# Performance work log

Hardware: AMD Instinct MI355X
Metric: run time of the kernel (lower is better)

Reference implementation:

```python
import jax, jax.numpy as jnp
import numpy as np

BATCH, SEQ, HEADS, EMB = 16, 4096, 16, 64
SHAPE = int(SEQ ** 0.5)          # 64 (2D grid side)
N = 2 * SHAPE - 1                # 127 (circular conv length)


def setup_inputs() -> dict:
    key = jax.random.key(0)
    k_v, k_w = jax.random.split(key)
    v = jax.random.normal(k_v, (BATCH, SEQ, HEADS, EMB), dtype=jnp.float32)
    # 'full' bias base: learned relative bias of length 2*shape_-1 per head
    w = jax.random.normal(k_w, (1, HEADS, N), dtype=jnp.float32)
    o_ = jnp.ones((SHAPE,), dtype=jnp.float32)
    return {"v": v, "w": w, "o_": o_}


def reference(v, w, o_):
    B, S, H, E = v.shape
    s = int(S ** 0.5)
    n = 2 * s - 1

    # bias_base_type == 'full': slice w[..., shape_-s : shape_+s-1] == all of w
    z_fft = jnp.fft.rfft(w)                              # (1, H, n//2+1) complex

    # v: [B, S, H, E] -> [B, E, H, s1, s2]
    vt = jnp.transpose(v, (0, 3, 2, 1)).reshape(B, E, H, s, s)
    v_s = vt.sum(axis=3)                                 # sum over s1 -> [B, E, H, s2]
    u_s = vt.sum(axis=4)                                 # sum over s2 -> [B, E, H, s1]

    pad = ((0, 0), (0, 0), (0, 0), (s - 1, 0))
    v_m_fft = jnp.fft.rfft(jnp.pad(v_s, pad))            # [B, E, H, n//2+1]
    u_m_fft = jnp.fft.rfft(jnp.pad(u_s, pad))

    zf = z_fft[:, None]                                  # (1, 1, H, n//2+1)
    RxV = jnp.fft.irfft(v_m_fft * zf, n=n)[..., :s]      # [B, E, H, s]
    RxU = jnp.fft.irfft(u_m_fft * zf, n=n)[..., :s]      # [B, E, H, s]

    # outer sum over the 2D grid, flatten back to seq
    pbv = RxV[..., None, :] + RxU[..., :, None]          # [B, E, H, s, s]
    pbv = pbv.reshape(B, E, H, S)
    pbv = jnp.transpose(pbv, (0, 3, 2, 1))               # [B, S, H, E]

    # normalizer term z_pb (batch independent)
    o_pad = jnp.pad(o_, ((s - 1, 0),))                   # (n,)
    o_fft = jnp.fft.rfft(o_pad)                          # (n//2+1,)
    z_pb = jnp.fft.irfft(o_fft * z_fft, n=n)[..., :s] * s  # (1, H, s)
    z_pb = z_pb[..., None, :] + z_pb[..., :, None]       # (1, H, s, s)
    z_pb = z_pb.reshape(-1, H, s * s)                    # (1, H, S)
    z_pb = jnp.transpose(z_pb, (0, 2, 1))                # (1, S, H)

    return pbv, z_pb
```

## Files before the change

### kernel.cpp

```cpp
#include <hip/hip_runtime.h>

#define BATCH 16
#define SEQ   4096
#define HEADS 16
#define EMB   64
#define SS    64
#define NW    127
#define PLANE (HEADS * EMB)

#define US_ELEMS    (BATCH * SS * PLANE)
#define VPART_ELEMS (BATCH * 4 * SS * PLANE)
#define WS_NEEDED ((size_t)(VPART_ELEMS + US_ELEMS) * sizeof(float))

__global__ __launch_bounds__(256) void sums_kernel(
    const float4* __restrict__ v4, float4* __restrict__ vpart4,
    float4* __restrict__ us4)
{
    __shared__ float4 u_lds[4][16][64];

    const int blk = blockIdx.x;
    const int b   = blk >> 4;
    const int q   = (blk >> 2) & 3;
    const int cq  = blk & 3;
    const int tid = threadIdx.x;
    const int w   = tid >> 6;
    const int c4  = tid & 63;

    const float4* base = v4 + (((size_t)(b * SEQ + q * 1024)) << 8)
                            + (cq << 6) + c4;

    float4 vacc[16];
    #pragma unroll
    for (int m = 0; m < 16; ++m) vacc[m] = make_float4(0.f, 0.f, 0.f, 0.f);

    for (int il = 0; il < 16; ++il) {
        float4 uacc = make_float4(0.f, 0.f, 0.f, 0.f);
        #pragma unroll
        for (int m = 0; m < 16; ++m) {
            const float4 x = base[(size_t)((il << 6) + w + (m << 2)) << 8];
            uacc.x += x.x; uacc.y += x.y; uacc.z += x.z; uacc.w += x.w;
            vacc[m].x += x.x; vacc[m].y += x.y;
            vacc[m].z += x.z; vacc[m].w += x.w;
        }
        u_lds[w][il][c4] = uacc;
    }
    __syncthreads();

    {
        int s = tid;
        #pragma unroll
        for (int r = 0; r < 4; ++r, s += 256) {
            const int il = s >> 6, c = s & 63;
            float4 a = u_lds[0][il][c];
            #pragma unroll
            for (int ww = 1; ww < 4; ++ww) {
                const float4 x = u_lds[ww][il][c];
                a.x += x.x; a.y += x.y; a.z += x.z; a.w += x.w;
            }
            us4[((size_t)((b << 6) + (q << 4) + il) << 8) + (cq << 6) + c] = a;
        }
    }

    #pragma unroll
    for (int m = 0; m < 16; ++m) {
        const int j = w + (m << 2);
        vpart4[((size_t)((((b << 2) + q) << 6) + j) << 8) + (cq << 6) + c4]
            = vacc[m];
    }
}

__global__ __launch_bounds__(512) void convexp_kernel(
    const float* __restrict__ w, const float4* __restrict__ vpart4,
    const float4* __restrict__ us4, float* __restrict__ out)
{
    __shared__ float wtab[NW];
    __shared__ float vsl[SS][SS];
    __shared__ float usl[SS][SS];

    const int bh   = blockIdx.x;
    const int b    = bh >> 4;
    const int h    = bh & (HEADS - 1);
    const int tid  = threadIdx.x;
    const int wave = tid >> 6;
    const int lane = tid & 63;

    if (tid < NW) wtab[tid] = w[h * NW + tid];

    for (int s = tid; s < SS * 16; s += 512) {
        const int j = s >> 4, e4 = s & 15;
        float4 acc = make_float4(0.f, 0.f, 0.f, 0.f);
        #pragma unroll
        for (int q = 0; q < 4; ++q) {
            const float4 x =
                vpart4[((size_t)((((b << 2) + q) << 6) + j) << 8) + (h << 4) + e4];
            acc.x += x.x; acc.y += x.y; acc.z += x.z; acc.w += x.w;
        }
        *(float4*)&vsl[j][e4 << 2] = acc;
        *(float4*)&usl[j][e4 << 2] =
            us4[((size_t)((b << 6) + j) << 8) + (h << 4) + e4];
    }
    __syncthreads();

    const int t0 = wave << 3;
    float accv[8], accu[8];
    #pragma unroll
    for (int tt = 0; tt < 8; ++tt) { accv[tt] = 0.0f; accu[tt] = 0.0f; }

    #pragma unroll
    for (int jb = 0; jb < 4; ++jb) {
        float wreg[23];
        #pragma unroll
        for (int d = 0; d < 23; ++d) {
            int idx = t0 - (jb << 4) + 49 + d;
            if (idx >= NW) idx -= NW;
            wreg[d] = wtab[idx];
        }
        #pragma unroll
        for (int jj = 0; jj < 16; ++jj) {
            const float cv = vsl[(jb << 4) + jj][lane];
            const float cu = usl[(jb << 4) + jj][lane];
            #pragma unroll
            for (int tt = 0; tt < 8; ++tt) {
                const float cw = wreg[15 + tt - jj];
                accv[tt] += cw * cv;
                accu[tt] += cw * cu;
            }
        }
    }
    __syncthreads();
    #pragma unroll
    for (int tt = 0; tt < 8; ++tt) {
        vsl[t0 + tt][lane] = accv[tt];
        usl[t0 + tt][lane] = accu[tt];
    }
    __syncthreads();

    float* obase = out + (((size_t)b * SEQ) << 10) + (h << 6) + lane;
    for (int ii = 0; ii < 8; ++ii) {
        const int i = (wave << 3) + ii;
        const float ruv = usl[i][lane];
        #pragma unroll
        for (int j = 0; j < SS; ++j) {
            obase[(size_t)((i << 6) + j) << 10] = vsl[j][lane] + ruv;
        }
    }
}

__global__ __launch_bounds__(512) void pbv_kernel(const float* __restrict__ v,
                                                  const float* __restrict__ w,
                                                  float* __restrict__ out) {
    __shared__ float us [SS][SS];
    __shared__ float vsf[SS][SS];
    __shared__ float wtab[NW];

    const int bh   = blockIdx.x;
    const int b    = bh / HEADS;
    const int h    = bh % HEADS;
    const int tid  = threadIdx.x;
    const int wave = tid >> 6;
    const int lane = tid & 63;

    for (int idx = tid; idx < SS * SS; idx += 512) (&vsf[0][0])[idx] = 0.0f;
    if (tid < NW) wtab[tid] = w[h * NW + tid];
    __syncthreads();

    const float* vbase = v + ((size_t)b * SEQ * HEADS + h) * EMB + lane;
    float vsacc[SS];
    #pragma unroll
    for (int j = 0; j < SS; ++j) vsacc[j] = 0.0f;

    for (int ii = 0; ii < 8; ++ii) {
        const int i = wave * 8 + ii;
        const float* rowp = vbase + (size_t)i * SS * (HEADS * EMB);
        float uacc = 0.0f;
        #pragma unroll
        for (int j = 0; j < SS; ++j) {
            float val = rowp[(size_t)j * (HEADS * EMB)];
            uacc += val;
            vsacc[j] += val;
        }
        us[i][lane] = uacc;
    }
    #pragma unroll
    for (int j = 0; j < SS; ++j) atomicAdd(&vsf[j][lane], vsacc[j]);
    __syncthreads();

    float rv[8], ru[8];
    for (int tt = 0; tt < 8; ++tt) {
        const int t = wave * 8 + tt;
        float accv = 0.0f, accu = 0.0f;
        #pragma unroll
        for (int j = 0; j < SS; ++j) {
            int k = t - j + 64;
            if (k >= NW) k -= NW;
            const float c = wtab[k];
            accv += c * vsf[j][lane];
            accu += c * us [j][lane];
        }
        rv[tt] = accv;
        ru[tt] = accu;
    }
    __syncthreads();
    for (int tt = 0; tt < 8; ++tt) {
        const int t = wave * 8 + tt;
        vsf[t][lane] = rv[tt];
        us [t][lane] = ru[tt];
    }
    __syncthreads();

    float* obase = out + ((size_t)b * SEQ * HEADS + h) * EMB + lane;
    for (int ii = 0; ii < 8; ++ii) {
        const int i = wave * 8 + ii;
        const float ruv = us[i][lane];
        #pragma unroll
        for (int j = 0; j < SS; ++j) {
            obase[(size_t)(i * SS + j) * (HEADS * EMB)] = vsf[j][lane] + ruv;
        }
    }
}

__global__ __launch_bounds__(256) void zpb_kernel(const float* __restrict__ w,
                                                  const float* __restrict__ o_,
                                                  float* __restrict__ out2) {
    __shared__ float zp[HEADS][SS];
    __shared__ float osh[SS];
    __shared__ float wsh[HEADS * NW];

    const int tid = threadIdx.x;
    const int g   = blockIdx.x;

    if (tid < SS) osh[tid] = o_[tid];
    for (int idx = tid; idx < HEADS * NW; idx += 256) wsh[idx] = w[idx];
    __syncthreads();

    for (int idx = tid; idx < HEADS * SS; idx += 256) {
        const int h = idx / SS, t = idx % SS;
        float acc = 0.0f;
        #pragma unroll
        for (int j = 0; j < SS; ++j) {
            int k = t - j + 64;
            if (k >= NW) k -= NW;
            acc += osh[j] * wsh[h * NW + k];
        }
        zp[h][t] = acc * (float)SS;
    }
    __syncthreads();

    for (int idx = tid; idx < SS * HEADS; idx += 256) {
        const int tl = idx / HEADS, h = idx % HEADS;
        out2[(size_t)(g * SS + tl) * HEADS + h] = zp[h][tl] + zp[h][g];
    }
}

extern "C" void kernel_launch(void* const* d_in, const int* in_sizes, int n_in,
                              void* d_out, int out_size, void* d_ws, size_t ws_size,
                              hipStream_t stream) {
    const float* v  = (const float*)d_in[0];
    const float* w  = (const float*)d_in[1];
    const float* o_ = (const float*)d_in[2];
    float* out = (float*)d_out;

    if (ws_size >= WS_NEEDED) {
        float* vpart = (float*)d_ws;
        float* us    = vpart + VPART_ELEMS;

        sums_kernel<<<256, 256, 0, stream>>>(
            (const float4*)v, (float4*)vpart, (float4*)us);
        convexp_kernel<<<BATCH * HEADS, 512, 0, stream>>>(
            w, (const float4*)vpart, (const float4*)us, out);
    } else {
        pbv_kernel<<<BATCH * HEADS, 512, 0, stream>>>(v, w, out);
    }

    const size_t out1_elems = (size_t)BATCH * SEQ * HEADS * EMB;
    zpb_kernel<<<SS, 256, 0, stream>>>(w, o_, out + out1_elems);
}
```

Baseline: 461.4 us.

## Split conv and expand into separate kernels with coalesced float4 output writes

Splits the fused convolution-plus-expansion kernel in two. The conv kernel now writes the RxV and RxU vectors to workspace. A new expand kernel, with one block per (batch, row), writes the 256 MB output using contiguous float4 stores instead of strided scalar stores from only 256 blocks. The sums kernel is also split finer (8 sequence quarters per batch, 512 blocks) to raise parallelism on the input read. The cost is an extra launch, a larger workspace and an extra round trip through global memory for the small intermediate vectors.

```diff
diff --git a/kernel.cpp b/kernel.cpp
--- a/kernel.cpp
+++ b/kernel.cpp
@@ -9,31 +9,31 @@
 #define PLANE (HEADS * EMB)
 
 #define US_ELEMS    (BATCH * SS * PLANE)
-#define VPART_ELEMS (BATCH * 4 * SS * PLANE)
-#define WS_NEEDED ((size_t)(VPART_ELEMS + US_ELEMS) * sizeof(float))
+#define VPART_ELEMS (BATCH * 8 * SS * PLANE)
+#define WS_NEEDED ((size_t)(VPART_ELEMS + 3 * US_ELEMS) * sizeof(float))
 
 __global__ __launch_bounds__(256) void sums_kernel(
     const float4* __restrict__ v4, float4* __restrict__ vpart4,
     float4* __restrict__ us4)
 {
-    __shared__ float4 u_lds[4][16][64];
+    __shared__ float4 u_lds[4][8][64];
 
     const int blk = blockIdx.x;
-    const int b   = blk >> 4;
-    const int q   = (blk >> 2) & 3;
+    const int b   = blk >> 5;
+    const int q   = (blk >> 2) & 7;
     const int cq  = blk & 3;
     const int tid = threadIdx.x;
     const int w   = tid >> 6;
     const int c4  = tid & 63;
 
-    const float4* base = v4 + (((size_t)(b * SEQ + q * 1024)) << 8)
+    const float4* base = v4 + (((size_t)(b * SEQ + q * 512)) << 8)
                             + (cq << 6) + c4;
 
     float4 vacc[16];
     #pragma unroll
     for (int m = 0; m < 16; ++m) vacc[m] = make_float4(0.f, 0.f, 0.f, 0.f);
 
-    for (int il = 0; il < 16; ++il) {
+    for (int il = 0; il < 8; ++il) {
         float4 uacc = make_float4(0.f, 0.f, 0.f, 0.f);
         #pragma unroll
         for (int m = 0; m < 16; ++m) {
@@ -49,7 +49,7 @@
     {
         int s = tid;
         #pragma unroll
-        for (int r = 0; r < 4; ++r, s += 256) {
+        for (int r = 0; r < 2; ++r, s += 256) {
             const int il = s >> 6, c = s & 63;
             float4 a = u_lds[0][il][c];
             #pragma unroll
@@ -57,21 +57,22 @@
                 const float4 x = u_lds[ww][il][c];
                 a.x += x.x; a.y += x.y; a.z += x.z; a.w += x.w;
             }
-            us4[((size_t)((b << 6) + (q << 4) + il) << 8) + (cq << 6) + c] = a;
+            us4[((size_t)((b << 6) + (q << 3) + il) << 8) + (cq << 6) + c] = a;
         }
     }
 
     #pragma unroll
     for (int m = 0; m < 16; ++m) {
         const int j = w + (m << 2);
-        vpart4[((size_t)((((b << 2) + q) << 6) + j) << 8) + (cq << 6) + c4]
+        vpart4[((size_t)((((b << 3) + q) << 6) + j) << 8) + (cq << 6) + c4]
             = vacc[m];
     }
 }
 
-__global__ __launch_bounds__(512) void convexp_kernel(
+__global__ __launch_bounds__(256) void conv_kernel(
     const float* __restrict__ w, const float4* __restrict__ vpart4,
-    const float4* __restrict__ us4, float* __restrict__ out)
+    const float4* __restrict__ us4, float* __restrict__ rxv,
+    float* __restrict__ rxu)
 {
     __shared__ float wtab[NW];
     __shared__ float vsl[SS][SS];
@@ -86,13 +87,13 @@
 
     if (tid < NW) wtab[tid] = w[h * NW + tid];
 
-    for (int s = tid; s < SS * 16; s += 512) {
+    for (int s = tid; s < SS * 16; s += 256) {
         const int j = s >> 4, e4 = s & 15;
         float4 acc = make_float4(0.f, 0.f, 0.f, 0.f);
         #pragma unroll
-        for (int q = 0; q < 4; ++q) {
+        for (int q = 0; q < 8; ++q) {
             const float4 x =
-                vpart4[((size_t)((((b << 2) + q) << 6) + j) << 8) + (h << 4) + e4];
+                vpart4[((size_t)((((b << 3) + q) << 6) + j) << 8) + (h << 4) + e4];
             acc.x += x.x; acc.y += x.y; acc.z += x.z; acc.w += x.w;
         }
         *(float4*)&vsl[j][e4 << 2] = acc;
@@ -101,48 +102,60 @@
     }
     __syncthreads();
 
-    const int t0 = wave << 3;
-    float accv[8], accu[8];
-    #pragma unroll
-    for (int tt = 0; tt < 8; ++tt) { accv[tt] = 0.0f; accu[tt] = 0.0f; }
+    const int t0 = wave * 16;
+    float accv[16], accu[16];
+    #pragma unroll
+    for (int tt = 0; tt < 16; ++tt) { accv[tt] = 0.0f; accu[tt] = 0.0f; }
 
     #pragma unroll
     for (int jb = 0; jb < 4; ++jb) {
-        float wreg[23];
-        #pragma unroll
-        for (int d = 0; d < 23; ++d) {
-            int idx = t0 - (jb << 4) + 49 + d;
+        float wreg[31];
+        #pragma unroll
+        for (int d = 0; d < 31; ++d) {
+            int idx = t0 - jb * 16 + 49 + d;
             if (idx >= NW) idx -= NW;
             wreg[d] = wtab[idx];
         }
         #pragma unroll
         for (int jj = 0; jj < 16; ++jj) {
-            const float cv = vsl[(jb << 4) + jj][lane];
-            const float cu = usl[(jb << 4) + jj][lane];
+            const float cv = vsl[jb * 16 + jj][lane];
+            const float cu = usl[jb * 16 + jj][lane];
             #pragma unroll
-            for (int tt = 0; tt < 8; ++tt) {
+            for (int tt = 0; tt < 16; ++tt) {
                 const float cw = wreg[15 + tt - jj];
                 accv[tt] += cw * cv;
                 accu[tt] += cw * cu;
             }
         }
     }
-    __syncthreads();
-    #pragma unroll
-    for (int tt = 0; tt < 8; ++tt) {
-        vsl[t0 + tt][lane] = accv[tt];
-        usl[t0 + tt][lane] = accu[tt];
-    }
-    __syncthreads();
-
-    float* obase = out + (((size_t)b * SEQ) << 10) + (h << 6) + lane;
-    for (int ii = 0; ii < 8; ++ii) {
-        const int i = (wave << 3) + ii;
-        const float ruv = usl[i][lane];
-        #pragma unroll
-        for (int j = 0; j < SS; ++j) {
-            obase[(size_t)((i << 6) + j) << 10] = vsl[j][lane] + ruv;
-        }
+
+    #pragma unroll
+    for (int tt = 0; tt < 16; ++tt) {
+        const size_t o = ((size_t)(b * SS + t0 + tt) << 10) + (h << 6) + lane;
+        rxv[o] = accv[tt];
+        rxu[o] = accu[tt];
+    }
+}
+
+__global__ __launch_bounds__(256) void expand_kernel(
+    const float* __restrict__ rxv, const float* __restrict__ rxu,
+    float* __restrict__ out)
+{
+    const int blk = blockIdx.x;
+    const int b   = blk >> 6;
+    const int tid = threadIdx.x;
+
+    const float4 ru = *((const float4*)(rxu + ((size_t)blk << 10)) + tid);
+    const float4* rvb = (const float4*)(rxv + ((size_t)b << 16));
+    float4* ob = (float4*)(out + (((size_t)blk) << 16)) + tid;
+
+    #pragma unroll 8
+    for (int j = 0; j < SS; ++j) {
+        float4 rv = rvb[(j << 8) + tid];
+        float4 r;
+        r.x = rv.x + ru.x; r.y = rv.y + ru.y;
+        r.z = rv.z + ru.z; r.w = rv.w + ru.w;
+        ob[(size_t)j << 8] = r;
     }
 }
 
@@ -263,11 +276,14 @@
     if (ws_size >= WS_NEEDED) {
         float* vpart = (float*)d_ws;
         float* us    = vpart + VPART_ELEMS;
-
-        sums_kernel<<<256, 256, 0, stream>>>(
+        float* rxv   = us    + US_ELEMS;
+        float* rxu   = rxv   + US_ELEMS;
+
+        sums_kernel<<<512, 256, 0, stream>>>(
             (const float4*)v, (float4*)vpart, (float4*)us);
-        convexp_kernel<<<BATCH * HEADS, 512, 0, stream>>>(
-            w, (const float4*)vpart, (const float4*)us, out);
+        conv_kernel<<<BATCH * HEADS, 256, 0, stream>>>(
+            w, (const float4*)vpart, (const float4*)us, rxv, rxu);
+        expand_kernel<<<BATCH * SS, 256, 0, stream>>>(rxv, rxu, out);
     } else {
         pbv_kernel<<<BATCH * HEADS, 512, 0, stream>>>(v, w, out);
     }
```

After: 481.5 us. 1.04x slower.
